# Kernel optimization log

Hardware: AMD Instinct MI355X
Metric: run time of the kernel (lower is better)

## Reference

```python
import jax, jax.numpy as jnp
import numpy as np

D_MODEL = 1024
N_HEADS = 16
WINDOW = 256
SEQ = 4096
BATCH = 1
NEG_INF = -1e30


def setup_inputs() -> dict:
    key = jax.random.key(0)
    ks = jax.random.split(key, 5)
    scale = 0.02
    inp = {"x": jax.random.normal(ks[0], (BATCH, SEQ, D_MODEL), jnp.float32)}
    for i, name in enumerate(["Wq", "Wk", "Wv", "Wo"]):
        inp[name] = jax.random.normal(ks[1 + i], (D_MODEL, D_MODEL), jnp.float32) * scale
    for name in ["bq", "bk", "bv", "bo"]:
        inp[name] = jnp.zeros((D_MODEL,), jnp.float32)
    return inp


def reference(x, Wq, bq, Wk, bk, Wv, bv, Wo, bo):
    B, S, D = x.shape
    H = N_HEADS
    hd = D // H
    # projections (torch Linear == x @ W^T + b; here W is stored pre-transposed)
    q = (x @ Wq + bq).reshape(B, S, H, hd).transpose(0, 2, 1, 3)  # [B,H,S,hd]
    k = (x @ Wk + bk).reshape(B, S, H, hd).transpose(0, 2, 1, 3)
    v = (x @ Wv + bv).reshape(B, S, H, hd).transpose(0, 2, 1, 3)
    scale = 1.0 / jnp.sqrt(jnp.asarray(hd, x.dtype))
    scores = jnp.einsum("bhqd,bhkd->bhqk", q, k) * scale  # [B,H,S,S]
    # causal sliding window: key j visible to query i iff 0 <= i - j < WINDOW
    i = jnp.arange(S)[:, None]
    j = jnp.arange(S)[None, :]
    allowed = (j <= i) & (i - j < WINDOW)  # [S,S]
    scores = jnp.where(allowed, scores, NEG_INF)
    attn = jax.nn.softmax(scores, axis=-1)
    out = jnp.einsum("bhqk,bhkd->bhqd", attn, v)  # [B,H,S,hd]
    out = out.transpose(0, 2, 1, 3).reshape(B, S, D)
    return out @ Wo + bo
```

## Files before the change

### kernel.cpp

```cpp
#include <hip/hip_runtime.h>
#include <hip/hip_bf16.h>


typedef __attribute__((ext_vector_type(8))) short bf16x8;
typedef __attribute__((ext_vector_type(4))) float f32x4;

#define S_LEN 4096
#define D_MODEL 1024
#define N_HEADS 16
#define HEAD_DIM 64
#define WINDOW 256
#define QKV_LD 3072

static __device__ __forceinline__ unsigned short f2bfbits(float f) {
    __hip_bfloat16 h = __float2bfloat16(f);
    unsigned short u;
    __builtin_memcpy(&u, &h, sizeof(u));
    return u;
}

typedef const __attribute__((address_space(1))) void c_gvoid;
typedef __attribute__((address_space(3))) void lvoid;
static __device__ __forceinline__ void gload16(const void* g, void* l) {
    __builtin_amdgcn_global_load_lds((c_gvoid*)g, (lvoid*)l, 16, 0, 0);
}

__global__ __launch_bounds__(256) void prep_k(const float* __restrict__ x,
                                              const float* __restrict__ Wq,
                                              const float* __restrict__ Wk,
                                              const float* __restrict__ Wv,
                                              const float* __restrict__ Wo,
                                              const float* __restrict__ bq,
                                              const float* __restrict__ bk,
                                              const float* __restrict__ bv,
                                              unsigned short* __restrict__ xb,
                                              __hip_bfloat16* __restrict__ Wqkvt,
                                              __hip_bfloat16* __restrict__ Wot,
                                              float* __restrict__ bias_cat) {
    const int b = blockIdx.x;
    const int t = threadIdx.x;
    if (b < 2048) {
        int i = b * 2048 + t * 8;
        float4 v0 = *(const float4*)(x + i);
        float4 v1 = *(const float4*)(x + i + 4);
        ushort4 o0, o1;
        o0.x = f2bfbits(v0.x); o0.y = f2bfbits(v0.y);
        o0.z = f2bfbits(v0.z); o0.w = f2bfbits(v0.w);
        o1.x = f2bfbits(v1.x); o1.y = f2bfbits(v1.y);
        o1.z = f2bfbits(v1.z); o1.w = f2bfbits(v1.w);
        *(ushort4*)(xb + i) = o0;
        *(ushort4*)(xb + i + 4) = o1;
        return;
    }
    if (b < 3072) {
        __shared__ __hip_bfloat16 tile[64][65];
        const int m = (b - 2048) >> 8;
        const int tid = (b - 2048) & 255;
        const int n0 = (tid & 15) * 64, k0 = (tid >> 4) * 64;
        const float* src = (m == 0) ? Wq : (m == 1) ? Wk : (m == 2) ? Wv : Wo;
        __hip_bfloat16* dst = (m < 3) ? (Wqkvt + (size_t)m * D_MODEL * D_MODEL) : Wot;
        for (int c = t; c < 1024; c += 256) {
            int r = c >> 4, c4 = (c & 15) * 4;
            float4 v = *(const float4*)(src + (size_t)(k0 + r) * D_MODEL + n0 + c4);
            tile[r][c4 + 0] = __float2bfloat16(v.x);
            tile[r][c4 + 1] = __float2bfloat16(v.y);
            tile[r][c4 + 2] = __float2bfloat16(v.z);
            tile[r][c4 + 3] = __float2bfloat16(v.w);
        }
        __syncthreads();
        for (int c = t; c < 1024; c += 256) {
            int rr = c >> 4, c4 = (c & 15) * 4;
            ushort4 o;
            unsigned short u0, u1, u2, u3;
            __builtin_memcpy(&u0, &tile[c4 + 0][rr], 2);
            __builtin_memcpy(&u1, &tile[c4 + 1][rr], 2);
            __builtin_memcpy(&u2, &tile[c4 + 2][rr], 2);
            __builtin_memcpy(&u3, &tile[c4 + 3][rr], 2);
            o.x = u0; o.y = u1; o.z = u2; o.w = u3;
            *(ushort4*)((unsigned short*)dst + (size_t)(n0 + rr) * D_MODEL + k0 + c4) = o;
        }
        return;
    }
    for (int c = t; c < 3 * D_MODEL; c += 256) {
        float v = (c < 1024) ? bq[c] : (c < 2048) ? bk[c - 1024] : bv[c - 2048];
        bias_cat[c] = v;
    }
}

__global__ __launch_bounds__(256, 2) void qkv_k(const __hip_bfloat16* __restrict__ A,
                                                const __hip_bfloat16* __restrict__ Bt,
                                                const float* __restrict__ bias,
                                                __hip_bfloat16* __restrict__ Cout) {
    constexpr int K = D_MODEL, N = QKV_LD;
    __shared__ __align__(16) char lds[2][40960];

    const int m0 = blockIdx.y * 128, n0 = blockIdx.x * 192;
    const int t = threadIdx.x;
    const int wave = t >> 6, lane = t & 63;
    const int quad = lane >> 4, l16 = lane & 15;
    const int wm = (wave & 1) * 64, wn = (wave >> 1) * 96;

    const int srow = t >> 3;
    const int scol = ((t & 7) ^ ((t >> 3) & 7)) * 8;

    f32x4 acc[4][6];
#pragma unroll
    for (int mi = 0; mi < 4; ++mi)
#pragma unroll
        for (int ni = 0; ni < 6; ++ni) acc[mi][ni] = (f32x4){0.f, 0.f, 0.f, 0.f};

    const __hip_bfloat16* gA = A + (size_t)(m0 + srow) * K + scol;
    const __hip_bfloat16* gB = Bt + (size_t)(n0 + srow) * K + scol;
    const int csw = ((quad ^ (l16 & 7)) << 4);

#define QSTAGE(WR, KT)                                                         \
    {                                                                          \
        const __hip_bfloat16* sa_ = gA + (KT) * 64;                            \
        const __hip_bfloat16* sb_ = gB + (KT) * 64;                            \
        char* da_ = &lds[WR][0] + t * 16;                                      \
        char* db_ = &lds[WR][16384] + t * 16;                                  \
        _Pragma("unroll") for (int p_ = 0; p_ < 4; ++p_)                       \
            gload16(sa_ + (size_t)(p_ * 32) * K, da_ + p_ * 4096);             \
        _Pragma("unroll") for (int p_ = 0; p_ < 6; ++p_)                       \
            gload16(sb_ + (size_t)(p_ * 32) * K, db_ + p_ * 4096);             \
    }

#define QITER(RD, WR, KT)                                                      \
    {                                                                          \
        bf16x8 af[4][2], bfr[6][2];                                            \
        const char* Ab_ = &lds[RD][0];                                         \
        const char* Bb_ = &lds[RD][16384];                                     \
        _Pragma("unroll") for (int mi = 0; mi < 4; ++mi) {                     \
            const char* pr = Ab_ + (wm + mi * 16 + l16) * 128;                 \
            af[mi][0] = *(const bf16x8*)(pr + csw);                            \
            af[mi][1] = *(const bf16x8*)(pr + (csw ^ 64));                     \
        }                                                                      \
        _Pragma("unroll") for (int ni = 0; ni < 6; ++ni) {                     \
            const char* pr = Bb_ + (wn + ni * 16 + l16) * 128;                 \
            bfr[ni][0] = *(const bf16x8*)(pr + csw);                           \
            bfr[ni][1] = *(const bf16x8*)(pr + (csw ^ 64));                    \
        }                                                                      \
        if ((KT) < 16) QSTAGE(WR, KT);                                         \
        asm volatile("s_waitcnt lgkmcnt(0)" ::: "memory");                     \
        __builtin_amdgcn_sched_barrier(0);                                     \
        __builtin_amdgcn_s_setprio(1);                                         \
        _Pragma("unroll") for (int kk = 0; kk < 2; ++kk)                       \
            _Pragma("unroll") for (int mi = 0; mi < 4; ++mi)                   \
                _Pragma("unroll") for (int ni = 0; ni < 6; ++ni)               \
                    acc[mi][ni] = __builtin_amdgcn_mfma_f32_16x16x32_bf16(     \
                        af[mi][kk], bfr[ni][kk], acc[mi][ni], 0, 0, 0);        \
        __builtin_amdgcn_s_setprio(0);                                         \
        __builtin_amdgcn_sched_barrier(0);                                     \
        asm volatile("s_waitcnt vmcnt(0)" ::: "memory");                       \
        __builtin_amdgcn_s_barrier();                                          \
    }

    QSTAGE(0, 0);
    asm volatile("s_waitcnt vmcnt(0)" ::: "memory");
    __builtin_amdgcn_s_barrier();

#pragma unroll 1
    for (int kt = 0; kt < 16; kt += 2) {
        QITER(0, 1, kt + 1);
        QITER(1, 0, kt + 2);
    }
#undef QITER
#undef QSTAGE

#pragma unroll
    for (int mi = 0; mi < 4; ++mi) {
#pragma unroll
        for (int ni = 0; ni < 6; ++ni) {
#pragma unroll
            for (int r = 0; r < 4; ++r) {
                int row = m0 + wm + mi * 16 + quad * 4 + r;
                int col = n0 + wn + ni * 16 + l16;
                float v = acc[mi][ni][r] + bias[col];
                Cout[(size_t)row * N + col] = __float2bfloat16(v);
            }
        }
    }
}

__global__ __launch_bounds__(256, 2) void wo_k(const __hip_bfloat16* __restrict__ A,
                                               const __hip_bfloat16* __restrict__ Bt,
                                               const float* __restrict__ bias,
                                               float* __restrict__ Cout) {
    constexpr int K = D_MODEL, N = D_MODEL;
    __shared__ __align__(16) char lds[2][24576];

    const int m0 = blockIdx.y * 128, n0 = blockIdx.x * 64;
    const int t = threadIdx.x;
    const int wave = t >> 6, lane = t & 63;
    const int quad = lane >> 4, l16 = lane & 15;
    const int wm = (wave & 1) * 64, wn = (wave >> 1) * 32;

    const int srow = t >> 3;
    const int scol = ((t & 7) ^ ((t >> 3) & 7)) * 8;

    f32x4 acc[4][2];
#pragma unroll
    for (int mi = 0; mi < 4; ++mi)
#pragma unroll
        for (int ni = 0; ni < 2; ++ni) acc[mi][ni] = (f32x4){0.f, 0.f, 0.f, 0.f};

    const __hip_bfloat16* gA = A + (size_t)(m0 + srow) * K + scol;
    const __hip_bfloat16* gB = Bt + (size_t)(n0 + srow) * K + scol;
    const int csw = ((quad ^ (l16 & 7)) << 4);

#define WSTAGE(WR, KT)                                                         \
    {                                                                          \
        const __hip_bfloat16* sa_ = gA + (KT) * 64;                            \
        const __hip_bfloat16* sb_ = gB + (KT) * 64;                            \
        char* da_ = &lds[WR][0] + t * 16;                                      \
        char* db_ = &lds[WR][16384] + t * 16;                                  \
        _Pragma("unroll") for (int p_ = 0; p_ < 4; ++p_)                       \
            gload16(sa_ + (size_t)(p_ * 32) * K, da_ + p_ * 4096);             \
        _Pragma("unroll") for (int p_ = 0; p_ < 2; ++p_)                       \
            gload16(sb_ + (size_t)(p_ * 32) * K, db_ + p_ * 4096);             \
    }

#define WITER(RD, WR, KT)                                                      \
    {                                                                          \
        bf16x8 af[4][2], bfr[2][2];                                            \
        const char* Ab_ = &lds[RD][0];                                         \
        const char* Bb_ = &lds[RD][16384];                                     \
        _Pragma("unroll") for (int mi = 0; mi < 4; ++mi) {                     \
            const char* pr = Ab_ + (wm + mi * 16 + l16) * 128;                 \
            af[mi][0] = *(const bf16x8*)(pr + csw);                            \
            af[mi][1] = *(const bf16x8*)(pr + (csw ^ 64));                     \
        }                                                                      \
        _Pragma("unroll") for (int ni = 0; ni < 2; ++ni) {                     \
            const char* pr = Bb_ + (wn + ni * 16 + l16) * 128;                 \
            bfr[ni][0] = *(const bf16x8*)(pr + csw);                           \
            bfr[ni][1] = *(const bf16x8*)(pr + (csw ^ 64));                    \
        }                                                                      \
        if ((KT) < 16) WSTAGE(WR, KT);                                         \
        asm volatile("s_waitcnt lgkmcnt(0)" ::: "memory");                     \
        __builtin_amdgcn_sched_barrier(0);                                     \
        __builtin_amdgcn_s_setprio(1);                                         \
        _Pragma("unroll") for (int kk = 0; kk < 2; ++kk)                       \
            _Pragma("unroll") for (int mi = 0; mi < 4; ++mi)                   \
                _Pragma("unroll") for (int ni = 0; ni < 2; ++ni)               \
                    acc[mi][ni] = __builtin_amdgcn_mfma_f32_16x16x32_bf16(     \
                        bfr[ni][kk], af[mi][kk], acc[mi][ni], 0, 0, 0);        \
        __builtin_amdgcn_s_setprio(0);                                         \
        __builtin_amdgcn_sched_barrier(0);                                     \
        asm volatile("s_waitcnt vmcnt(0)" ::: "memory");                       \
        __builtin_amdgcn_s_barrier();                                          \
    }

    WSTAGE(0, 0);
    asm volatile("s_waitcnt vmcnt(0)" ::: "memory");
    __builtin_amdgcn_s_barrier();

#pragma unroll 1
    for (int kt = 0; kt < 16; kt += 2) {
        WITER(0, 1, kt + 1);
        WITER(1, 0, kt + 2);
    }
#undef WITER
#undef WSTAGE

    float4 bv[2];
#pragma unroll
    for (int ni = 0; ni < 2; ++ni)
        bv[ni] = *(const float4*)&bias[n0 + wn + ni * 16 + quad * 4];
#pragma unroll
    for (int mi = 0; mi < 4; ++mi) {
        const int row = m0 + wm + mi * 16 + l16;
#pragma unroll
        for (int ni = 0; ni < 2; ++ni) {
            const int col = n0 + wn + ni * 16 + quad * 4;
            float4 o;
            o.x = acc[mi][ni][0] + bv[ni].x;
            o.y = acc[mi][ni][1] + bv[ni].y;
            o.z = acc[mi][ni][2] + bv[ni].z;
            o.w = acc[mi][ni][3] + bv[ni].w;
            *(float4*)(Cout + (size_t)row * N + col) = o;
        }
    }
}

__global__ __launch_bounds__(256) void attn_k(const __hip_bfloat16* __restrict__ QKV,
                                              __hip_bfloat16* __restrict__ AO) {
    __shared__ __align__(16) __hip_bfloat16 Qs[128 * 64];
    __shared__ __align__(16) __hip_bfloat16 Ks[2][64 * 64];
    __shared__ __align__(16) __hip_bfloat16 Vt[2][64 * 72];
    __shared__ __align__(16) __hip_bfloat16 Ps[128 * 72];

    const int h = blockIdx.y;
    const int i0 = blockIdx.x * 128;
    const int t = threadIdx.x;
    const int wave = t >> 6, lane = t & 63;
    const int quad = lane >> 4, l16 = lane & 15;
    const float sc = 0.125f * 1.44269504088896f;

    const __hip_bfloat16* Q = QKV + h * HEAD_DIM;
    const __hip_bfloat16* K = QKV + D_MODEL + h * HEAD_DIM;
    const __hip_bfloat16* V = QKV + 2 * D_MODEL + h * HEAD_DIM;

    const int grow = t >> 3;
    const int glog = ((t & 7) ^ ((t >> 3) & 7)) * 8;
    const int vp = t >> 3, vc = t & 7;

    const int tt0 = (i0 >= WINDOW) ? 0 : ((WINDOW - i0) >> 6);

#pragma unroll
    for (int p = 0; p < 4; ++p)
        gload16(Q + (size_t)(i0 + p * 32 + grow) * QKV_LD + glog,
                &Qs[p * 2048 + t * 8]);
    {
        const int tb0 = i0 - WINDOW + tt0 * 64;
        uint4 pv0 = *(const uint4*)(V + (size_t)(tb0 + 2 * vp) * QKV_LD + vc * 8);
        uint4 pv1 = *(const uint4*)(V + (size_t)(tb0 + 2 * vp + 1) * QKV_LD + vc * 8);
#pragma unroll
        for (int p = 0; p < 2; ++p)
            gload16(K + (size_t)(tb0 + p * 32 + grow) * QKV_LD + glog,
                    &Ks[0][p * 2048 + t * 8]);
        const unsigned short* a0 = (const unsigned short*)&pv0;
        const unsigned short* a1 = (const unsigned short*)&pv1;
#pragma unroll
        for (int j = 0; j < 8; ++j) {
            unsigned int pk = (unsigned int)a0[j] | ((unsigned int)a1[j] << 16);
            *(unsigned int*)&Vt[0][(vc * 8 + j) * 72 + 2 * vp] = pk;
        }
    }
    __syncthreads();

    const int rq0 = wave * 32 + l16;
    bf16x8 aq[2][2];
#pragma unroll
    for (int m = 0; m < 2; ++m) {
        const int rq = rq0 + m * 16;
#pragma unroll
        for (int kk = 0; kk < 2; ++kk)
            aq[m][kk] = *(const bf16x8*)&Qs[rq * 64 + ((kk * 4 + quad) ^ (rq & 7)) * 8];
    }

    float m_i[2] = {-3.0e38f, -3.0e38f}, l_i[2] = {0.f, 0.f};
    f32x4 Ov[2][4];
#pragma unroll
    for (int m = 0; m < 2; ++m)
#pragma unroll
        for (int no = 0; no < 4; ++no) Ov[m][no] = (f32x4){0.f, 0.f, 0.f, 0.f};

    for (int tt = tt0; tt < 6; ++tt) {
        const int tb = i0 - WINDOW + tt * 64;
        const int buf = (tt - tt0) & 1;

        f32x4 s[2][4];
#pragma unroll
        for (int m = 0; m < 2; ++m)
#pragma unroll
            for (int ni = 0; ni < 4; ++ni) s[m][ni] = (f32x4){0.f, 0.f, 0.f, 0.f};
        __builtin_amdgcn_s_setprio(1);
#pragma unroll
        for (int kk = 0; kk < 2; ++kk)
#pragma unroll
            for (int ni = 0; ni < 4; ++ni) {
                int rk = ni * 16 + l16;
                bf16x8 bk = *(const bf16x8*)&Ks[buf][rk * 64 + ((kk * 4 + quad) ^ (rk & 7)) * 8];
#pragma unroll
                for (int m = 0; m < 2; ++m)
                    s[m][ni] = __builtin_amdgcn_mfma_f32_16x16x32_bf16(
                        bk, aq[m][kk], s[m][ni], 0, 0, 0);
            }
        __builtin_amdgcn_s_setprio(0);

        const bool pf = (tt < 5);
        uint4 nv0, nv1;
        if (pf) {
            const int tbn = tb + 64;
            nv0 = *(const uint4*)(V + (size_t)(tbn + 2 * vp) * QKV_LD + vc * 8);
            nv1 = *(const uint4*)(V + (size_t)(tbn + 2 * vp + 1) * QKV_LD + vc * 8);
#pragma unroll
            for (int p = 0; p < 2; ++p)
                gload16(K + (size_t)(tbn + p * 32 + grow) * QKV_LD + glog,
                        &Ks[buf ^ 1][p * 2048 + t * 8]);
        }

#pragma unroll
        for (int m = 0; m < 2; ++m) {
            const int qi = i0 + rq0 + m * 16;
            float mx = -3.0e38f;
#pragma unroll
            for (int ni = 0; ni < 4; ++ni)
#pragma unroll
                for (int r = 0; r < 4; ++r) {
                    int j = tb + ni * 16 + quad * 4 + r;
                    float v = s[m][ni][r] * sc;
                    bool ok = (j <= qi) && (qi - j < WINDOW);
                    v = ok ? v : -3.0e38f;
                    s[m][ni][r] = v;
                    mx = fmaxf(mx, v);
                }
            mx = fmaxf(mx, __shfl_xor(mx, 16));
            mx = fmaxf(mx, __shfl_xor(mx, 32));
            const float mn = fmaxf(m_i[m], mx);
            const float alpha = exp2f(m_i[m] - mn);
            m_i[m] = mn;
            float sum = 0.f;
#pragma unroll
            for (int ni = 0; ni < 4; ++ni)
#pragma unroll
                for (int r = 0; r < 4; ++r) {
                    float e = exp2f(s[m][ni][r] - mn);
                    s[m][ni][r] = e;
                    sum += e;
                }
            sum += __shfl_xor(sum, 16);
            sum += __shfl_xor(sum, 32);
            l_i[m] = l_i[m] * alpha + sum;
#pragma unroll
            for (int no = 0; no < 4; ++no) Ov[m][no] *= alpha;

            const int rq = rq0 + m * 16;
#pragma unroll
            for (int ni = 0; ni < 4; ++ni) {
                ushort4 w4;
                w4.x = f2bfbits(s[m][ni][0]); w4.y = f2bfbits(s[m][ni][1]);
                w4.z = f2bfbits(s[m][ni][2]); w4.w = f2bfbits(s[m][ni][3]);
                *(ushort4*)&Ps[rq * 72 + ni * 16 + quad * 4] = w4;
            }
        }

        __builtin_amdgcn_s_setprio(1);
#pragma unroll
        for (int kk = 0; kk < 2; ++kk) {
            bf16x8 ap[2];
#pragma unroll
            for (int m = 0; m < 2; ++m)
                ap[m] = *(const bf16x8*)&Ps[(rq0 + m * 16) * 72 + kk * 32 + quad * 8];
#pragma unroll
            for (int no = 0; no < 4; ++no) {
                bf16x8 bvv = *(const bf16x8*)&Vt[buf][(no * 16 + l16) * 72 + kk * 32 + quad * 8];
#pragma unroll
                for (int m = 0; m < 2; ++m)
                    Ov[m][no] = __builtin_amdgcn_mfma_f32_16x16x32_bf16(
                        bvv, ap[m], Ov[m][no], 0, 0, 0);
            }
        }
        __builtin_amdgcn_s_setprio(0);

        if (pf) {
            const unsigned short* a0 = (const unsigned short*)&nv0;
            const unsigned short* a1 = (const unsigned short*)&nv1;
#pragma unroll
            for (int j = 0; j < 8; ++j) {
                unsigned int pk = (unsigned int)a0[j] | ((unsigned int)a1[j] << 16);
                *(unsigned int*)&Vt[buf ^ 1][(vc * 8 + j) * 72 + 2 * vp] = pk;
            }
        }
        __syncthreads();
    }

#pragma unroll
    for (int m = 0; m < 2; ++m) {
        const float inv = 1.0f / l_i[m];
        const int qi = i0 + rq0 + m * 16;
#pragma unroll
        for (int no = 0; no < 4; ++no) {
            ushort4 o;
            o.x = f2bfbits(Ov[m][no][0] * inv);
            o.y = f2bfbits(Ov[m][no][1] * inv);
            o.z = f2bfbits(Ov[m][no][2] * inv);
            o.w = f2bfbits(Ov[m][no][3] * inv);
            *(ushort4*)((unsigned short*)AO + (size_t)qi * D_MODEL + h * HEAD_DIM +
                        no * 16 + quad * 4) = o;
        }
    }
}

extern "C" void kernel_launch(void* const* d_in, const int* in_sizes, int n_in,
                              void* d_out, int out_size, void* d_ws, size_t ws_size,
                              hipStream_t stream) {
    const float* x  = (const float*)d_in[0];
    const float* Wq = (const float*)d_in[1];
    const float* Wk = (const float*)d_in[2];
    const float* Wv = (const float*)d_in[3];
    const float* Wo = (const float*)d_in[4];
    const float* bq = (const float*)d_in[5];
    const float* bk = (const float*)d_in[6];
    const float* bv = (const float*)d_in[7];
    const float* bo = (const float*)d_in[8];
    float* out = (float*)d_out;

    char* w = (char*)d_ws;
    const size_t MB = 1u << 20;
    __hip_bfloat16* xb    = (__hip_bfloat16*)(w + 0 * MB);
    __hip_bfloat16* Wqkvt = (__hip_bfloat16*)(w + 8 * MB);
    __hip_bfloat16* Wot   = (__hip_bfloat16*)(w + 14 * MB);
    float*          bcat  = (float*)(w + 16 * MB);
    __hip_bfloat16* QKV   = (__hip_bfloat16*)(w + 17 * MB);
    __hip_bfloat16* AO    = (__hip_bfloat16*)(w + 41 * MB);

    prep_k<<<3073, 256, 0, stream>>>(x, Wq, Wk, Wv, Wo, bq, bk, bv,
                                     (unsigned short*)xb, Wqkvt, Wot, bcat);

    dim3 gqkv(QKV_LD / 192, S_LEN / 128);
    qkv_k<<<gqkv, 256, 0, stream>>>(xb, Wqkvt, bcat, QKV);

    dim3 ag(S_LEN / 128, N_HEADS);
    attn_k<<<ag, 256, 0, stream>>>(QKV, AO);

    dim3 go(D_MODEL / 64, S_LEN / 128);
    wo_k<<<go, 256, 0, stream>>>(AO, Wot, bo, out);
}
```

Baseline: 160.0 us.

## Deepen QKV GEMM pipeline to four stages with smaller K tiles

The QKV projection GEMM now uses four LDS buffers with a K tile of 32 instead of two buffers with a K tile of 64, keeping two stages of global-to-LDS loads in flight. The wait before each barrier becomes a partial vmcnt wait, so the next stage's loads can stay outstanding. The XOR swizzle on LDS columns is dropped for a plain 64-byte row layout. The aim is to hide global memory latency better, at the cost of more barriers per K step, fewer MFMAs per barrier, and possible LDS bank conflicts on fragment reads. Issuing a stage two iterations ahead also risks an LDS buffer being overwritten while slower waves are still reading it.

```diff
diff --git a/kernel.cpp b/kernel.cpp
--- a/kernel.cpp
+++ b/kernel.cpp
@@ -92,7 +92,7 @@
                                                 const float* __restrict__ bias,
                                                 __hip_bfloat16* __restrict__ Cout) {
     constexpr int K = D_MODEL, N = QKV_LD;
-    __shared__ __align__(16) char lds[2][40960];
+    __shared__ __align__(16) char lds[4 * 20480];
 
     const int m0 = blockIdx.y * 128, n0 = blockIdx.x * 192;
     const int t = threadIdx.x;
@@ -100,8 +100,8 @@
     const int quad = lane >> 4, l16 = lane & 15;
     const int wm = (wave & 1) * 64, wn = (wave >> 1) * 96;
 
-    const int srow = t >> 3;
-    const int scol = ((t & 7) ^ ((t >> 3) & 7)) * 8;
+    const int srow = t >> 2;
+    const int scol = (t & 3) * 8;
 
     f32x4 acc[4][6];
 #pragma unroll
@@ -111,58 +111,51 @@
 
     const __hip_bfloat16* gA = A + (size_t)(m0 + srow) * K + scol;
     const __hip_bfloat16* gB = Bt + (size_t)(n0 + srow) * K + scol;
-    const int csw = ((quad ^ (l16 & 7)) << 4);
 
 #define QSTAGE(WR, KT)                                                         \
     {                                                                          \
-        const __hip_bfloat16* sa_ = gA + (KT) * 64;                            \
-        const __hip_bfloat16* sb_ = gB + (KT) * 64;                            \
-        char* da_ = &lds[WR][0] + t * 16;                                      \
-        char* db_ = &lds[WR][16384] + t * 16;                                  \
-        _Pragma("unroll") for (int p_ = 0; p_ < 4; ++p_)                       \
-            gload16(sa_ + (size_t)(p_ * 32) * K, da_ + p_ * 4096);             \
-        _Pragma("unroll") for (int p_ = 0; p_ < 6; ++p_)                       \
-            gload16(sb_ + (size_t)(p_ * 32) * K, db_ + p_ * 4096);             \
+        const __hip_bfloat16* sa_ = gA + (KT) * 32;                            \
+        const __hip_bfloat16* sb_ = gB + (KT) * 32;                            \
+        char* da_ = lds + (WR) * 20480 + t * 16;                               \
+        char* db_ = lds + (WR) * 20480 + 8192 + t * 16;                        \
+        _Pragma("unroll") for (int p_ = 0; p_ < 2; ++p_)                       \
+            gload16(sa_ + (size_t)(p_ * 64) * K, da_ + p_ * 4096);             \
+        _Pragma("unroll") for (int p_ = 0; p_ < 3; ++p_)                       \
+            gload16(sb_ + (size_t)(p_ * 64) * K, db_ + p_ * 4096);             \
     }
 
 #define QITER(RD, WR, KT)                                                      \
     {                                                                          \
-        bf16x8 af[4][2], bfr[6][2];                                            \
-        const char* Ab_ = &lds[RD][0];                                         \
-        const char* Bb_ = &lds[RD][16384];                                     \
-        _Pragma("unroll") for (int mi = 0; mi < 4; ++mi) {                     \
-            const char* pr = Ab_ + (wm + mi * 16 + l16) * 128;                 \
-            af[mi][0] = *(const bf16x8*)(pr + csw);                            \
-            af[mi][1] = *(const bf16x8*)(pr + (csw ^ 64));                     \
-        }                                                                      \
-        _Pragma("unroll") for (int ni = 0; ni < 6; ++ni) {                     \
-            const char* pr = Bb_ + (wn + ni * 16 + l16) * 128;                 \
-            bfr[ni][0] = *(const bf16x8*)(pr + csw);                           \
-            bfr[ni][1] = *(const bf16x8*)(pr + (csw ^ 64));                    \
-        }                                                                      \
-        if ((KT) < 16) QSTAGE(WR, KT);                                         \
-        asm volatile("s_waitcnt lgkmcnt(0)" ::: "memory");                     \
-        __builtin_amdgcn_sched_barrier(0);                                     \
+        bf16x8 af[4], bfr[6];                                                  \
+        const char* Ab_ = lds + (RD) * 20480;                                  \
+        const char* Bb_ = Ab_ + 8192;                                          \
+        _Pragma("unroll") for (int mi = 0; mi < 4; ++mi)                       \
+            af[mi] = *(const bf16x8*)(Ab_ + (wm + mi * 16 + l16) * 64 + quad * 16); \
+        _Pragma("unroll") for (int ni = 0; ni < 6; ++ni)                       \
+            bfr[ni] = *(const bf16x8*)(Bb_ + (wn + ni * 16 + l16) * 64 + quad * 16); \
+        if ((KT) < 32) QSTAGE(WR, KT);                                         \
         __builtin_amdgcn_s_setprio(1);                                         \
-        _Pragma("unroll") for (int kk = 0; kk < 2; ++kk)                       \
-            _Pragma("unroll") for (int mi = 0; mi < 4; ++mi)                   \
-                _Pragma("unroll") for (int ni = 0; ni < 6; ++ni)               \
-                    acc[mi][ni] = __builtin_amdgcn_mfma_f32_16x16x32_bf16(     \
-                        af[mi][kk], bfr[ni][kk], acc[mi][ni], 0, 0, 0);        \
+        _Pragma("unroll") for (int mi = 0; mi < 4; ++mi)                       \
+            _Pragma("unroll") for (int ni = 0; ni < 6; ++ni)                   \
+                acc[mi][ni] = __builtin_amdgcn_mfma_f32_16x16x32_bf16(         \
+                    af[mi], bfr[ni], acc[mi][ni], 0, 0, 0);                    \
         __builtin_amdgcn_s_setprio(0);                                         \
-        __builtin_amdgcn_sched_barrier(0);                                     \
-        asm volatile("s_waitcnt vmcnt(0)" ::: "memory");                       \
+        if ((KT) < 32) { asm volatile("s_waitcnt vmcnt(5)" ::: "memory"); }    \
+        else           { asm volatile("s_waitcnt vmcnt(0)" ::: "memory"); }    \
         __builtin_amdgcn_s_barrier();                                          \
     }
 
     QSTAGE(0, 0);
-    asm volatile("s_waitcnt vmcnt(0)" ::: "memory");
+    QSTAGE(1, 1);
+    asm volatile("s_waitcnt vmcnt(5)" ::: "memory");
     __builtin_amdgcn_s_barrier();
 
 #pragma unroll 1
-    for (int kt = 0; kt < 16; kt += 2) {
-        QITER(0, 1, kt + 1);
-        QITER(1, 0, kt + 2);
+    for (int kt = 0; kt < 32; kt += 4) {
+        QITER(0, 2, kt + 2);
+        QITER(1, 3, kt + 3);
+        QITER(2, 0, kt + 4);
+        QITER(3, 1, kt + 5);
     }
 #undef QITER
 #undef QSTAGE
```

Measured after the change: 162.4 us. Within noise of the previous version (+1.5%).
